# Performance work log

Measured on AMD Instinct MI355X. Metric: run time of the kernel, lower is better.

Reference implementation:

```python
import jax, jax.numpy as jnp
import numpy as np

EPS = 1e-5  # torch BatchNorm1d default eps

N_NODES = 100000
N_EDGES = 1250000
N_GRAPHS = 512
F_IN = 16
HID = 64


def _bn(x, w, b):
    # track_running_stats=False, momentum=None -> always batch statistics (biased var)
    m = jnp.mean(x, axis=0)
    v = jnp.var(x, axis=0)
    return (x - m) * jax.lax.rsqrt(v + EPS) * w + b


def _prelu(x, a):
    return jnp.where(x >= 0, x, a * x)


def _gcn_conv(x, W, b, src, dst, n):
    # PyG GCNConv: h = x W; add self loops; sym-norm by deg^-1/2 on target degrees
    h = x @ W  # [N, out]
    ones = jnp.ones(src.shape[0], x.dtype)
    deg = jax.ops.segment_sum(ones, dst, num_segments=n) + 1.0  # +1 self loop
    dis = jax.lax.rsqrt(deg)  # deg >= 1 so finite
    norm = (dis[src] * dis[dst])[:, None]  # [E,1]
    agg = jax.ops.segment_sum(h[src] * norm, dst, num_segments=n)
    # self-loop contribution: norm = dis[i]*dis[i]
    return agg + h * (dis * dis)[:, None] + b


def setup_inputs() -> dict:
    key = jax.random.key(0)
    ks = jax.random.split(key, 12)
    x = jax.random.normal(ks[0], (N_NODES, F_IN), dtype=jnp.float32)
    edge_index = jax.random.randint(ks[1], (2, N_EDGES), 0, N_NODES, dtype=jnp.int32)
    # evenly spaced graph ids so every segment is non-empty (global_max_pool)
    batch = ((jnp.arange(N_NODES, dtype=jnp.int32) * N_GRAPHS) // N_NODES).astype(jnp.int32)
    s = 0.1
    W1 = jax.random.normal(ks[2], (F_IN, HID), jnp.float32) * s
    b1 = jnp.zeros((HID,), jnp.float32)
    W2 = jax.random.normal(ks[3], (HID, HID), jnp.float32) * s
    b2 = jnp.zeros((HID,), jnp.float32)
    lw1 = jax.random.normal(ks[4], (HID, HID), jnp.float32) * s
    lb1 = jnp.zeros((HID,), jnp.float32)
    lw2 = jax.random.normal(ks[5], (HID, 1), jnp.float32) * s
    lb2 = jnp.zeros((1,), jnp.float32)
    bn1_w = jnp.ones((HID,), jnp.float32); bn1_b = jnp.zeros((HID,), jnp.float32)
    bn2_w = jnp.ones((HID,), jnp.float32); bn2_b = jnp.zeros((HID,), jnp.float32)
    bn3_w = jnp.ones((HID,), jnp.float32); bn3_b = jnp.zeros((HID,), jnp.float32)
    bn4_w = jnp.ones((1,), jnp.float32); bn4_b = jnp.zeros((1,), jnp.float32)
    a1 = jnp.full((1,), 0.25, jnp.float32)
    a2 = jnp.full((1,), 0.25, jnp.float32)
    a3 = jnp.full((1,), 0.25, jnp.float32)
    a4 = jnp.full((1,), 0.25, jnp.float32)
    return {"x": x, "edge_index": edge_index, "batch": batch,
            "W1": W1, "b1": b1, "W2": W2, "b2": b2,
            "bn1_w": bn1_w, "bn1_b": bn1_b, "bn2_w": bn2_w, "bn2_b": bn2_b,
            "bn3_w": bn3_w, "bn3_b": bn3_b, "bn4_w": bn4_w, "bn4_b": bn4_b,
            "lw1": lw1, "lb1": lb1, "lw2": lw2, "lb2": lb2,
            "a1": a1, "a2": a2, "a3": a3, "a4": a4}


def reference(x, edge_index, batch, W1, b1, W2, b2,
              bn1_w, bn1_b, bn2_w, bn2_b, bn3_w, bn3_b, bn4_w, bn4_b,
              lw1, lb1, lw2, lb2, a1, a2, a3, a4):
    src, dst = edge_index[0], edge_index[1]
    n = x.shape[0]
    h = _gcn_conv(x, W1, b1, src, dst, n)
    h = _prelu(_bn(h, bn1_w, bn1_b), a1)
    h = _gcn_conv(h, W2, b2, src, dst, n)
    h = _prelu(_bn(h, bn2_w, bn2_b), a2)
    g = jax.ops.segment_max(h, batch, num_segments=N_GRAPHS)  # global_max_pool
    g = _prelu(_bn(g @ lw1 + lb1, bn3_w, bn3_b), a3)
    g = _prelu(_bn(g @ lw2 + lb2, bn4_w, bn4_b), a4)
    return g
```

## Files before the change

### kernel.cpp

```cpp
#include <hip/hip_runtime.h>
#include <hip/hip_bf16.h>

#define N_NODES 100000
#define N_EDGES 1250000
#define N_GRAPHS 512
#define F_IN 16
#define HID 64
#define EPS 1e-5f

#define K_B 1563
#define B_H 250
#define EPB 5000
#define M_SC (K_B * B_H)

typedef unsigned int uint;

__device__ __forceinline__ uint f2bf(float f) {
    uint u = __float_as_uint(f);
    return (u + 0x7fffu + ((u >> 16) & 1u)) >> 16;
}
__device__ __forceinline__ uint pack2(float lo, float hi) {
    return f2bf(lo) | (f2bf(hi) << 16);
}
__device__ __forceinline__ void unpack8(float* o, uint4 v) {
    o[0] = __uint_as_float(v.x << 16); o[1] = __uint_as_float(v.x & 0xffff0000u);
    o[2] = __uint_as_float(v.y << 16); o[3] = __uint_as_float(v.y & 0xffff0000u);
    o[4] = __uint_as_float(v.z << 16); o[5] = __uint_as_float(v.z & 0xffff0000u);
    o[6] = __uint_as_float(v.w << 16); o[7] = __uint_as_float(v.w & 0xffff0000u);
}
__device__ __forceinline__ void accum8(float* a, uint4 v) {
    a[0] += __uint_as_float(v.x << 16); a[1] += __uint_as_float(v.x & 0xffff0000u);
    a[2] += __uint_as_float(v.y << 16); a[3] += __uint_as_float(v.y & 0xffff0000u);
    a[4] += __uint_as_float(v.z << 16); a[5] += __uint_as_float(v.z & 0xffff0000u);
    a[6] += __uint_as_float(v.w << 16); a[7] += __uint_as_float(v.w & 0xffff0000u);
}


__global__ __launch_bounds__(256) void k_hist(const int4* __restrict__ dst4,
                                              int* __restrict__ hist) {
    __shared__ int h[K_B];
    int t = threadIdx.x, b = blockIdx.x;
    for (int k = t; k < K_B; k += 256) h[k] = 0;
    __syncthreads();
    const int4* d4 = dst4 + b * (EPB / 4);
    for (int i = t; i < EPB / 4; i += 256) {
        int4 d = d4[i];
        atomicAdd(&h[d.x >> 6], 1);
        atomicAdd(&h[d.y >> 6], 1);
        atomicAdd(&h[d.z >> 6], 1);
        atomicAdd(&h[d.w >> 6], 1);
    }
    __syncthreads();
    for (int k = t; k < K_B; k += 256) hist[k * B_H + b] = h[k];
}

__global__ void k_s1(const int* __restrict__ in, int* __restrict__ out,
                     int* __restrict__ bsum, int n) {
    __shared__ int sh[256];
    int blk = blockIdx.x, t = threadIdx.x;
    int base = blk * 1024 + t * 4;
    int v[4];
#pragma unroll
    for (int j = 0; j < 4; j++) { int i = base + j; v[j] = (i < n) ? in[i] : 0; }
    int tsum = v[0] + v[1] + v[2] + v[3];
    sh[t] = tsum;
    __syncthreads();
    for (int ofs = 1; ofs < 256; ofs <<= 1) {
        int x = (t >= ofs) ? sh[t - ofs] : 0;
        __syncthreads();
        sh[t] += x;
        __syncthreads();
    }
    int run = sh[t] - tsum;
    if (t == 255) bsum[blk] = sh[255];
#pragma unroll
    for (int j = 0; j < 4; j++) { int i = base + j; if (i < n) out[i] = run; run += v[j]; }
}

__global__ void k_s2(int* __restrict__ bsum, int nb) {
    __shared__ int sh[512];
    int t = threadIdx.x;
    int v = (t < nb) ? bsum[t] : 0;
    sh[t] = v;
    __syncthreads();
    for (int ofs = 1; ofs < 512; ofs <<= 1) {
        int x = (t >= ofs) ? sh[t - ofs] : 0;
        __syncthreads();
        sh[t] += x;
        __syncthreads();
    }
    if (t < nb) bsum[t] = sh[t] - v;
}

__global__ void k_s3(int* __restrict__ out, const int* __restrict__ bsum, int n) {
    int i = blockIdx.x * 256 + threadIdx.x;
    if (i < n) out[i] += bsum[i >> 10];
}

__global__ __launch_bounds__(256) void k_bucketize(const int4* __restrict__ src4,
        const int4* __restrict__ dst4, const int* __restrict__ ebase,
        int* __restrict__ ebuck) {
    __shared__ int base[K_B];
    int t = threadIdx.x, b = blockIdx.x;
    for (int k = t; k < K_B; k += 256) base[k] = ebase[k * B_H + b];
    __syncthreads();
    const int4* s4 = src4 + b * (EPB / 4);
    const int4* d4 = dst4 + b * (EPB / 4);
    for (int i = t; i < EPB / 4; i += 256) {
        int4 s = s4[i];
        int4 d = d4[i];
        int p;
        p = atomicAdd(&base[d.x >> 6], 1); ebuck[p] = s.x | ((d.x & 63) << 17);
        p = atomicAdd(&base[d.y >> 6], 1); ebuck[p] = s.y | ((d.y & 63) << 17);
        p = atomicAdd(&base[d.z >> 6], 1); ebuck[p] = s.z | ((d.z & 63) << 17);
        p = atomicAdd(&base[d.w >> 6], 1); ebuck[p] = s.w | ((d.w & 63) << 17);
    }
}

__global__ __launch_bounds__(256) void k_csr(const int* __restrict__ ebase,
        const int* __restrict__ ebuck, int* __restrict__ col,
        int2* __restrict__ meta, float* __restrict__ dis) {
    int k = blockIdx.x, t = threadIdx.x;
    int beg = ebase[k * B_H];
    int end = (k + 1 < K_B) ? ebase[(k + 1) * B_H] : N_EDGES;
    int m = end - beg;
    __shared__ int c[64];
    __shared__ int sb[64];
    if (t < 64) c[t] = 0;
    __syncthreads();
    for (int i = t; i < m; i += 256) atomicAdd(&c[ebuck[beg + i] >> 17], 1);
    __syncthreads();
    if (t < 64) {
        int v = c[t];
        int incl = v;
#pragma unroll
        for (int o = 1; o < 64; o <<= 1) { int u = __shfl_up(incl, o); if (t >= o) incl += u; }
        int excl = incl - v;
        int node = k * 64 + t;
        if (node < N_NODES) {
            meta[node] = make_int2(beg + excl, v);
            dis[node] = rsqrtf((float)v + 1.0f);
        }
        sb[t] = beg + excl;
    }
    __syncthreads();
    for (int i = t; i < m; i += 256) {
        int e = ebuck[beg + i];
        int pos = atomicAdd(&sb[e >> 17], 1);
        col[pos] = e & 0x1FFFF;
    }
}


__global__ __launch_bounds__(512) void k_gemm1(const float* __restrict__ x,
        const float* __restrict__ W1, const float* __restrict__ dis,
        ushort* __restrict__ A) {
    __shared__ float Ws[F_IN * HID];
    __shared__ float xs[32 * F_IN];
    int t = threadIdx.x;
    Ws[t] = W1[t];
    Ws[t + 512] = W1[t + 512];
    int n0 = blockIdx.x * 32;
    xs[t] = x[n0 * F_IN + t];
    __syncthreads();
    int f = t & 63, w = t >> 6;
    float Wreg[F_IN];
#pragma unroll
    for (int k = 0; k < F_IN; k++) Wreg[k] = Ws[k * HID + f];
#pragma unroll
    for (int i = 0; i < 4; i++) {
        int nl = w * 4 + i;
        float acc = 0.f;
#pragma unroll
        for (int kq = 0; kq < 4; kq++) {
            const float4 xv = *(const float4*)&xs[nl * F_IN + kq * 4];
            acc = fmaf(xv.x, Wreg[4 * kq + 0], acc);
            acc = fmaf(xv.y, Wreg[4 * kq + 1], acc);
            acc = fmaf(xv.z, Wreg[4 * kq + 2], acc);
            acc = fmaf(xv.w, Wreg[4 * kq + 3], acc);
        }
        int n = n0 + nl;
        A[(size_t)n * HID + f] = (ushort)f2bf(acc * dis[n]);
    }
}

__global__ __launch_bounds__(512) void k_gemm2(const ushort* __restrict__ B,
        const float* __restrict__ scale, const float* __restrict__ shift,
        const float* __restrict__ alpha, const float* __restrict__ W2,
        const float* __restrict__ dis, ushort* __restrict__ A2) {
    __shared__ float Ws[HID * HID];
    __shared__ float xs[32 * HID];
    int t = threadIdx.x;
#pragma unroll
    for (int i = 0; i < 8; i++) Ws[i * 512 + t] = W2[i * 512 + t];
    int n0 = blockIdx.x * 32;
    float al = alpha[0];
    {
        const uint* Bu = (const uint*)(B + (size_t)n0 * HID);
#pragma unroll
        for (int i = 0; i < 2; i++) {
            int idx = i * 512 + t;
            uint u = Bu[idx];
            int fp = (idx & 31) * 2;
            int row = idx >> 5;
            float lo = __uint_as_float(u << 16) * scale[fp] + shift[fp];
            float hi = __uint_as_float(u & 0xffff0000u) * scale[fp + 1] + shift[fp + 1];
            lo = lo >= 0.f ? lo : al * lo;
            hi = hi >= 0.f ? hi : al * hi;
            xs[row * HID + fp] = lo;
            xs[row * HID + fp + 1] = hi;
        }
    }
    __syncthreads();
    int f = t & 63, w = t >> 6;
    float Wreg[HID];
#pragma unroll
    for (int k = 0; k < HID; k++) Wreg[k] = Ws[k * HID + f];
#pragma unroll
    for (int i = 0; i < 4; i++) {
        int nl = w * 4 + i;
        float acc = 0.f;
#pragma unroll
        for (int kq = 0; kq < 16; kq++) {
            const float4 xv = *(const float4*)&xs[nl * HID + kq * 4];
            acc = fmaf(xv.x, Wreg[4 * kq + 0], acc);
            acc = fmaf(xv.y, Wreg[4 * kq + 1], acc);
            acc = fmaf(xv.z, Wreg[4 * kq + 2], acc);
            acc = fmaf(xv.w, Wreg[4 * kq + 3], acc);
        }
        int n = n0 + nl;
        A2[(size_t)n * HID + f] = (ushort)f2bf(acc * dis[n]);
    }
}

__global__ __launch_bounds__(256) void k_agg(const uint4* __restrict__ Asc,
        const float* __restrict__ dis, const int2* __restrict__ meta,
        const int* __restrict__ col, const float* __restrict__ bias,
        uint4* __restrict__ outB) {
    int t = threadIdx.x;
    int nid = blockIdx.x * 32 + (t >> 3);
    int fq = t & 7;
    int2 mt = meta[nid];
    int beg = mt.x, m = mt.y;
    float acc[8] = {0, 0, 0, 0, 0, 0, 0, 0};
    int j = 0;
    for (; j + 2 <= m; j += 2) {
        int s0 = col[beg + j];
        int s1 = col[beg + j + 1];
        uint4 r0 = Asc[(size_t)s0 * 8 + fq];
        uint4 r1 = Asc[(size_t)s1 * 8 + fq];
        accum8(acc, r0);
        accum8(acc, r1);
    }
    if (j < m) {
        int s = col[beg + j];
        accum8(acc, Asc[(size_t)s * 8 + fq]);
    }
    accum8(acc, Asc[(size_t)nid * 8 + fq]);
    float dn = dis[nid];
    float4 b0 = ((const float4*)bias)[fq * 2];
    float4 b1 = ((const float4*)bias)[fq * 2 + 1];
    float o0 = b0.x + dn * acc[0], o1 = b0.y + dn * acc[1];
    float o2 = b0.z + dn * acc[2], o3 = b0.w + dn * acc[3];
    float o4 = b1.x + dn * acc[4], o5 = b1.y + dn * acc[5];
    float o6 = b1.z + dn * acc[6], o7 = b1.w + dn * acc[7];
    uint4 ov;
    ov.x = pack2(o0, o1); ov.y = pack2(o2, o3);
    ov.z = pack2(o4, o5); ov.w = pack2(o6, o7);
    outB[(size_t)nid * 8 + fq] = ov;
}

__global__ __launch_bounds__(256) void k_stats(const uint4* __restrict__ a,
        float* __restrict__ sum, float* __restrict__ sumsq) {
    int t = threadIdx.x, rg = t >> 3, fq = t & 7;
    float s[8] = {0, 0, 0, 0, 0, 0, 0, 0}, q[8] = {0, 0, 0, 0, 0, 0, 0, 0};
    for (int r = blockIdx.x * 32 + rg; r < N_NODES; r += gridDim.x * 32) {
        float o[8];
        unpack8(o, a[(size_t)r * 8 + fq]);
#pragma unroll
        for (int i = 0; i < 8; i++) { s[i] += o[i]; q[i] += o[i] * o[i]; }
    }
    __shared__ float shs[2048], shq[2048];
#pragma unroll
    for (int i = 0; i < 8; i++) {
        shs[rg * 64 + fq * 8 + i] = s[i];
        shq[rg * 64 + fq * 8 + i] = q[i];
    }
    __syncthreads();
    if (t < 64) {
        float ts = 0, tq = 0;
#pragma unroll
        for (int i = 0; i < 32; i++) { ts += shs[i * 64 + t]; tq += shq[i * 64 + t]; }
        atomicAdd(&sum[t], ts);
        atomicAdd(&sumsq[t], tq);
    }
}

__global__ void k_bnfin(const float* __restrict__ sum, const float* __restrict__ sumsq,
                        const float* __restrict__ w, const float* __restrict__ b,
                        float* __restrict__ scale, float* __restrict__ shift, float invn) {
    int f = threadIdx.x;
    float m = sum[f] * invn;
    float v = sumsq[f] * invn - m * m;
    float sc = w[f] * rsqrtf(v + EPS);
    scale[f] = sc;
    shift[f] = b[f] - m * sc;
}

__global__ __launch_bounds__(256) void k_pool(const uint4* __restrict__ a,
        const float* __restrict__ scale, const float* __restrict__ shift,
        const float* __restrict__ alpha, float* __restrict__ g) {
    int gi = blockIdx.x;
    int lo = (gi * N_NODES + N_GRAPHS - 1) / N_GRAPHS;
    int hi = ((gi + 1) * N_NODES + N_GRAPHS - 1) / N_GRAPHS;
    int t = threadIdx.x, rg = t >> 3, fq = t & 7;
    float al = alpha[0];
    float4 c0 = ((const float4*)scale)[fq * 2], c1 = ((const float4*)scale)[fq * 2 + 1];
    float4 d0 = ((const float4*)shift)[fq * 2], d1 = ((const float4*)shift)[fq * 2 + 1];
    float sc[8] = {c0.x, c0.y, c0.z, c0.w, c1.x, c1.y, c1.z, c1.w};
    float sh[8] = {d0.x, d0.y, d0.z, d0.w, d1.x, d1.y, d1.z, d1.w};
    float mx[8];
#pragma unroll
    for (int i = 0; i < 8; i++) mx[i] = -INFINITY;
    for (int r = lo + rg; r < hi; r += 32) {
        float o[8];
        unpack8(o, a[(size_t)r * 8 + fq]);
#pragma unroll
        for (int i = 0; i < 8; i++) {
            float v = o[i] * sc[i] + sh[i];
            v = v >= 0.f ? v : al * v;
            mx[i] = fmaxf(mx[i], v);
        }
    }
    __shared__ float sm[2048];
#pragma unroll
    for (int i = 0; i < 8; i++) sm[rg * 64 + fq * 8 + i] = mx[i];
    __syncthreads();
    if (t < 64) {
        float m = sm[t];
#pragma unroll
        for (int i = 1; i < 32; i++) m = fmaxf(m, sm[i * 64 + t]);
        g[gi * HID + t] = m;
    }
}

__global__ void k_lin1(const float* __restrict__ g, const float* __restrict__ lw1,
                       const float* __restrict__ lb1, float* __restrict__ t1,
                       float* __restrict__ s3, float* __restrict__ ss3) {
    __shared__ float row[HID];
    int r = blockIdx.x, f = threadIdx.x;
    row[f] = g[r * HID + f];
    __syncthreads();
    float acc = lb1[f];
#pragma unroll
    for (int k = 0; k < HID; k++) acc += row[k] * lw1[k * HID + f];
    t1[r * HID + f] = acc;
    atomicAdd(&s3[f], acc);
    atomicAdd(&ss3[f], acc * acc);
}

__global__ void k_lin2(const float* __restrict__ t1, const float* __restrict__ s3,
                       const float* __restrict__ ss3, const float* __restrict__ bn3w,
                       const float* __restrict__ bn3b, const float* __restrict__ a3,
                       const float* __restrict__ lw2, const float* __restrict__ lb2,
                       float* __restrict__ t2, float* __restrict__ s4) {
    int r = blockIdx.x, f = threadIdx.x;
    const float invn = 1.f / N_GRAPHS;
    float m = s3[f] * invn;
    float v = ss3[f] * invn - m * m;
    float sc = bn3w[f] * rsqrtf(v + EPS);
    float x = (t1[r * HID + f] - m) * sc + bn3b[f];
    float al = a3[0];
    x = (x >= 0.f) ? x : al * x;
    float p = x * lw2[f];
    for (int o = 32; o > 0; o >>= 1) p += __shfl_down(p, o);
    if (f == 0) {
        float tv = p + lb2[0];
        t2[r] = tv;
        atomicAdd(&s4[0], tv);
        atomicAdd(&s4[1], tv * tv);
    }
}

__global__ void k_final(const float* __restrict__ t2, const float* __restrict__ s4,
                        const float* __restrict__ bn4w, const float* __restrict__ bn4b,
                        const float* __restrict__ a4, float* __restrict__ out) {
    int r = threadIdx.x;
    const float invn = 1.f / N_GRAPHS;
    float m = s4[0] * invn;
    float v = s4[1] * invn - m * m;
    float sc = bn4w[0] * rsqrtf(v + EPS);
    float x = (t2[r] - m) * sc + bn4b[0];
    float al = a4[0];
    out[r] = (x >= 0.f) ? x : al * x;
}

extern "C" void kernel_launch(void* const* d_in, const int* in_sizes, int n_in,
                              void* d_out, int out_size, void* d_ws, size_t ws_size,
                              hipStream_t stream) {
    const float* x   = (const float*)d_in[0];
    const int*   ei  = (const int*)d_in[1];
    const int4*  src4 = (const int4*)ei;
    const int4*  dst4 = (const int4*)(ei + N_EDGES);
    const float* W1  = (const float*)d_in[3];
    const float* b1  = (const float*)d_in[4];
    const float* W2  = (const float*)d_in[5];
    const float* b2  = (const float*)d_in[6];
    const float* bn1w = (const float*)d_in[7];
    const float* bn1b = (const float*)d_in[8];
    const float* bn2w = (const float*)d_in[9];
    const float* bn2b = (const float*)d_in[10];
    const float* bn3w = (const float*)d_in[11];
    const float* bn3b = (const float*)d_in[12];
    const float* bn4w = (const float*)d_in[13];
    const float* bn4b = (const float*)d_in[14];
    const float* lw1  = (const float*)d_in[15];
    const float* lb1  = (const float*)d_in[16];
    const float* lw2  = (const float*)d_in[17];
    const float* lb2  = (const float*)d_in[18];
    const float* a1   = (const float*)d_in[19];
    const float* a2   = (const float*)d_in[20];
    const float* a3   = (const float*)d_in[21];
    const float* a4   = (const float*)d_in[22];
    float* out = (float*)d_out;

    char* p = (char*)d_ws;
    auto carve = [&](size_t bytes) -> void* {
        void* r = (void*)p;
        p += (bytes + 255) & ~(size_t)255;
        return r;
    };
    int*    hist = (int*)carve((size_t)M_SC * 4);
    int*    ebase = (int*)carve((size_t)M_SC * 4);
    int*    ebuck = (int*)carve((size_t)N_EDGES * 4);
    int*    col  = (int*)carve((size_t)N_EDGES * 4);
    float*  dis  = (float*)carve((size_t)N_NODES * 4);
    int2*   meta = (int2*)carve((size_t)N_NODES * 8);
    int*    bsum = (int*)carve(2048);
    ushort* A    = (ushort*)carve((size_t)N_NODES * HID * 2);
    ushort* B    = (ushort*)carve((size_t)N_NODES * HID * 2);
    float*  gbuf = (float*)carve((size_t)N_GRAPHS * HID * 4);
    float*  t1   = (float*)carve((size_t)N_GRAPHS * HID * 4);
    float*  t2   = (float*)carve((size_t)N_GRAPHS * 4);
    float*  stats = (float*)carve(16 * HID * 4);
    float* s1 = stats,        *ss1 = stats + 64;
    float* sc1 = stats + 128, *sh1 = stats + 192;
    float* s2 = stats + 256,  *ss2 = stats + 320;
    float* sc2 = stats + 384, *sh2 = stats + 448;
    float* s3 = stats + 512,  *ss3 = stats + 576;
    float* s4 = stats + 640;

    hipMemsetAsync(stats, 0, 16 * HID * 4, stream);

    const int SC_BLKS = (M_SC + 1023) / 1024;

    k_hist<<<B_H, 256, 0, stream>>>(dst4, hist);
    k_s1<<<SC_BLKS, 256, 0, stream>>>(hist, ebase, bsum, M_SC);
    k_s2<<<1, 512, 0, stream>>>(bsum, SC_BLKS);
    k_s3<<<(M_SC + 255) / 256, 256, 0, stream>>>(ebase, bsum, M_SC);
    k_bucketize<<<B_H, 256, 0, stream>>>(src4, dst4, ebase, ebuck);
    k_csr<<<K_B, 256, 0, stream>>>(ebase, ebuck, col, meta, dis);

    const int NB32 = N_NODES / 32;
    k_gemm1<<<NB32, 512, 0, stream>>>(x, W1, dis, A);
    k_agg<<<NB32, 256, 0, stream>>>((const uint4*)A, dis, meta, col, b1, (uint4*)B);
    k_stats<<<512, 256, 0, stream>>>((const uint4*)B, s1, ss1);
    k_bnfin<<<1, 64, 0, stream>>>(s1, ss1, bn1w, bn1b, sc1, sh1, 1.f / N_NODES);
    k_gemm2<<<NB32, 512, 0, stream>>>(B, sc1, sh1, a1, W2, dis, A);
    k_agg<<<NB32, 256, 0, stream>>>((const uint4*)A, dis, meta, col, b2, (uint4*)B);
    k_stats<<<512, 256, 0, stream>>>((const uint4*)B, s2, ss2);
    k_bnfin<<<1, 64, 0, stream>>>(s2, ss2, bn2w, bn2b, sc2, sh2, 1.f / N_NODES);
    k_pool<<<N_GRAPHS, 256, 0, stream>>>((const uint4*)B, sc2, sh2, a2, gbuf);
    k_lin1<<<N_GRAPHS, 64, 0, stream>>>(gbuf, lw1, lb1, t1, s3, ss3);
    k_lin2<<<N_GRAPHS, 64, 0, stream>>>(t1, s3, ss3, bn3w, bn3b, a3, lw2, lb2, t2, s4);
    k_final<<<1, N_GRAPHS, 0, stream>>>(t2, s4, bn4w, bn4b, a4, out);
}
```

Measured before the change: 208.9 us.

## Fuse BN stats into aggregation, fold scan fixup and head kernels

Removes the k_s3 scan-fixup pass by adding the block offsets inside bucketize and csr. BatchNorm sum and sum-of-squares are now reduced inside k_agg and written to 8 replicated atomic slots, which drops the separate stats and bnfin kernels. BN finalisation is recomputed per block in gemm2 and pool. The lin1 layer is folded into pool, and lin2 plus the final BN go into a single head kernel. The aggregation loop is unrolled to 4 edges. Together this cuts several kernel launches and one full re-read of the node features, at the cost of atomics and redundant per-block BN finalisation.

```diff
diff --git a/kernel.cpp b/kernel.cpp
--- a/kernel.cpp
+++ b/kernel.cpp
@@ -92,17 +92,15 @@
     if (t < nb) bsum[t] = sh[t] - v;
 }
 
-__global__ void k_s3(int* __restrict__ out, const int* __restrict__ bsum, int n) {
-    int i = blockIdx.x * 256 + threadIdx.x;
-    if (i < n) out[i] += bsum[i >> 10];
-}
-
 __global__ __launch_bounds__(256) void k_bucketize(const int4* __restrict__ src4,
         const int4* __restrict__ dst4, const int* __restrict__ ebase,
-        int* __restrict__ ebuck) {
+        const int* __restrict__ bsum, int* __restrict__ ebuck) {
     __shared__ int base[K_B];
     int t = threadIdx.x, b = blockIdx.x;
-    for (int k = t; k < K_B; k += 256) base[k] = ebase[k * B_H + b];
+    for (int k = t; k < K_B; k += 256) {
+        int idx = k * B_H + b;
+        base[k] = ebase[idx] + bsum[idx >> 10];
+    }
     __syncthreads();
     const int4* s4 = src4 + b * (EPB / 4);
     const int4* d4 = dst4 + b * (EPB / 4);
@@ -118,11 +116,18 @@
 }
 
 __global__ __launch_bounds__(256) void k_csr(const int* __restrict__ ebase,
-        const int* __restrict__ ebuck, int* __restrict__ col,
-        int2* __restrict__ meta, float* __restrict__ dis) {
+        const int* __restrict__ bsum, const int* __restrict__ ebuck,
+        int* __restrict__ col, int2* __restrict__ meta, float* __restrict__ dis) {
     int k = blockIdx.x, t = threadIdx.x;
-    int beg = ebase[k * B_H];
-    int end = (k + 1 < K_B) ? ebase[(k + 1) * B_H] : N_EDGES;
+    int i0 = k * B_H;
+    int beg = ebase[i0] + bsum[i0 >> 10];
+    int end;
+    if (k + 1 < K_B) {
+        int i1 = (k + 1) * B_H;
+        end = ebase[i1] + bsum[i1 >> 10];
+    } else {
+        end = N_EDGES;
+    }
     int m = end - beg;
     __shared__ int c[64];
     __shared__ int sb[64];
@@ -185,14 +190,28 @@
 }
 
 __global__ __launch_bounds__(512) void k_gemm2(const ushort* __restrict__ B,
-        const float* __restrict__ scale, const float* __restrict__ shift,
+        const float* __restrict__ s1r, const float* __restrict__ ss1r,
+        const float* __restrict__ bnw, const float* __restrict__ bnb,
         const float* __restrict__ alpha, const float* __restrict__ W2,
         const float* __restrict__ dis, ushort* __restrict__ A2) {
     __shared__ float Ws[HID * HID];
     __shared__ float xs[32 * HID];
+    __shared__ float scs[64], shsv[64];
     int t = threadIdx.x;
 #pragma unroll
     for (int i = 0; i < 8; i++) Ws[i * 512 + t] = W2[i * 512 + t];
+    if (t < 64) {
+        float s = 0, q = 0;
+#pragma unroll
+        for (int r = 0; r < 8; r++) { s += s1r[r * 64 + t]; q += ss1r[r * 64 + t]; }
+        const float invn = 1.f / N_NODES;
+        float m = s * invn;
+        float v = q * invn - m * m;
+        float sc = bnw[t] * rsqrtf(v + EPS);
+        scs[t] = sc;
+        shsv[t] = bnb[t] - m * sc;
+    }
+    __syncthreads();
     int n0 = blockIdx.x * 32;
     float al = alpha[0];
     {
@@ -203,8 +222,8 @@
             uint u = Bu[idx];
             int fp = (idx & 31) * 2;
             int row = idx >> 5;
-            float lo = __uint_as_float(u << 16) * scale[fp] + shift[fp];
-            float hi = __uint_as_float(u & 0xffff0000u) * scale[fp + 1] + shift[fp + 1];
+            float lo = __uint_as_float(u << 16) * scs[fp] + shsv[fp];
+            float hi = __uint_as_float(u & 0xffff0000u) * scs[fp + 1] + shsv[fp + 1];
             lo = lo >= 0.f ? lo : al * lo;
             hi = hi >= 0.f ? hi : al * hi;
             xs[row * HID + fp] = lo;
@@ -236,7 +255,8 @@
 __global__ __launch_bounds__(256) void k_agg(const uint4* __restrict__ Asc,
         const float* __restrict__ dis, const int2* __restrict__ meta,
         const int* __restrict__ col, const float* __restrict__ bias,
-        uint4* __restrict__ outB) {
+        uint4* __restrict__ outB, float* __restrict__ sumr,
+        float* __restrict__ sumsqr) {
     int t = threadIdx.x;
     int nid = blockIdx.x * 32 + (t >> 3);
     int fq = t & 7;
@@ -244,15 +264,21 @@
     int beg = mt.x, m = mt.y;
     float acc[8] = {0, 0, 0, 0, 0, 0, 0, 0};
     int j = 0;
-    for (; j + 2 <= m; j += 2) {
+    for (; j + 4 <= m; j += 4) {
         int s0 = col[beg + j];
         int s1 = col[beg + j + 1];
+        int s2 = col[beg + j + 2];
+        int s3 = col[beg + j + 3];
         uint4 r0 = Asc[(size_t)s0 * 8 + fq];
         uint4 r1 = Asc[(size_t)s1 * 8 + fq];
+        uint4 r2 = Asc[(size_t)s2 * 8 + fq];
+        uint4 r3 = Asc[(size_t)s3 * 8 + fq];
         accum8(acc, r0);
         accum8(acc, r1);
-    }
-    if (j < m) {
+        accum8(acc, r2);
+        accum8(acc, r3);
+    }
+    for (; j < m; ++j) {
         int s = col[beg + j];
         accum8(acc, Asc[(size_t)s * 8 + fq]);
     }
@@ -260,65 +286,75 @@
     float dn = dis[nid];
     float4 b0 = ((const float4*)bias)[fq * 2];
     float4 b1 = ((const float4*)bias)[fq * 2 + 1];
-    float o0 = b0.x + dn * acc[0], o1 = b0.y + dn * acc[1];
-    float o2 = b0.z + dn * acc[2], o3 = b0.w + dn * acc[3];
-    float o4 = b1.x + dn * acc[4], o5 = b1.y + dn * acc[5];
-    float o6 = b1.z + dn * acc[6], o7 = b1.w + dn * acc[7];
+    float o[8];
+    o[0] = b0.x + dn * acc[0]; o[1] = b0.y + dn * acc[1];
+    o[2] = b0.z + dn * acc[2]; o[3] = b0.w + dn * acc[3];
+    o[4] = b1.x + dn * acc[4]; o[5] = b1.y + dn * acc[5];
+    o[6] = b1.z + dn * acc[6]; o[7] = b1.w + dn * acc[7];
     uint4 ov;
-    ov.x = pack2(o0, o1); ov.y = pack2(o2, o3);
-    ov.z = pack2(o4, o5); ov.w = pack2(o6, o7);
+    ov.x = pack2(o[0], o[1]); ov.y = pack2(o[2], o[3]);
+    ov.z = pack2(o[4], o[5]); ov.w = pack2(o[6], o[7]);
     outB[(size_t)nid * 8 + fq] = ov;
-}
-
-__global__ __launch_bounds__(256) void k_stats(const uint4* __restrict__ a,
-        float* __restrict__ sum, float* __restrict__ sumsq) {
+
+    float sq[8];
+#pragma unroll
+    for (int i = 0; i < 8; i++) sq[i] = o[i] * o[i];
+#pragma unroll
+    for (int ofs = 8; ofs <= 32; ofs <<= 1) {
+#pragma unroll
+        for (int i = 0; i < 8; i++) {
+            o[i] += __shfl_xor(o[i], ofs);
+            sq[i] += __shfl_xor(sq[i], ofs);
+        }
+    }
+    __shared__ float ps[4][64], pq[4][64];
+    int w = t >> 6, lane = t & 63;
+    if (lane < 8) {
+#pragma unroll
+        for (int i = 0; i < 8; i++) {
+            ps[w][lane * 8 + i] = o[i];
+            pq[w][lane * 8 + i] = sq[i];
+        }
+    }
+    __syncthreads();
+    if (t < 64) {
+        float a = ps[0][t] + ps[1][t] + ps[2][t] + ps[3][t];
+        float b = pq[0][t] + pq[1][t] + pq[2][t] + pq[3][t];
+        int rep = (blockIdx.x & 7) * 64;
+        atomicAdd(&sumr[rep + t], a);
+        atomicAdd(&sumsqr[rep + t], b);
+    }
+}
+
+__global__ __launch_bounds__(256) void k_pool(const uint4* __restrict__ a,
+        const float* __restrict__ s2r, const float* __restrict__ ss2r,
+        const float* __restrict__ bnw, const float* __restrict__ bnb,
+        const float* __restrict__ alpha, const float* __restrict__ lw1,
+        const float* __restrict__ lb1, float* __restrict__ th,
+        float* __restrict__ s3r, float* __restrict__ ss3r) {
+    __shared__ float scs[64], shsv[64];
+    __shared__ float sm[2048];
+    __shared__ float gr[64];
+    int gi = blockIdx.x;
     int t = threadIdx.x, rg = t >> 3, fq = t & 7;
-    float s[8] = {0, 0, 0, 0, 0, 0, 0, 0}, q[8] = {0, 0, 0, 0, 0, 0, 0, 0};
-    for (int r = blockIdx.x * 32 + rg; r < N_NODES; r += gridDim.x * 32) {
-        float o[8];
-        unpack8(o, a[(size_t)r * 8 + fq]);
-#pragma unroll
-        for (int i = 0; i < 8; i++) { s[i] += o[i]; q[i] += o[i] * o[i]; }
-    }
-    __shared__ float shs[2048], shq[2048];
-#pragma unroll
-    for (int i = 0; i < 8; i++) {
-        shs[rg * 64 + fq * 8 + i] = s[i];
-        shq[rg * 64 + fq * 8 + i] = q[i];
-    }
-    __syncthreads();
     if (t < 64) {
-        float ts = 0, tq = 0;
-#pragma unroll
-        for (int i = 0; i < 32; i++) { ts += shs[i * 64 + t]; tq += shq[i * 64 + t]; }
-        atomicAdd(&sum[t], ts);
-        atomicAdd(&sumsq[t], tq);
-    }
-}
-
-__global__ void k_bnfin(const float* __restrict__ sum, const float* __restrict__ sumsq,
-                        const float* __restrict__ w, const float* __restrict__ b,
-                        float* __restrict__ scale, float* __restrict__ shift, float invn) {
-    int f = threadIdx.x;
-    float m = sum[f] * invn;
-    float v = sumsq[f] * invn - m * m;
-    float sc = w[f] * rsqrtf(v + EPS);
-    scale[f] = sc;
-    shift[f] = b[f] - m * sc;
-}
-
-__global__ __launch_bounds__(256) void k_pool(const uint4* __restrict__ a,
-        const float* __restrict__ scale, const float* __restrict__ shift,
-        const float* __restrict__ alpha, float* __restrict__ g) {
-    int gi = blockIdx.x;
+        float s = 0, q = 0;
+#pragma unroll
+        for (int r = 0; r < 8; r++) { s += s2r[r * 64 + t]; q += ss2r[r * 64 + t]; }
+        const float invn = 1.f / N_NODES;
+        float m = s * invn;
+        float v = q * invn - m * m;
+        float sc = bnw[t] * rsqrtf(v + EPS);
+        scs[t] = sc;
+        shsv[t] = bnb[t] - m * sc;
+    }
+    __syncthreads();
     int lo = (gi * N_NODES + N_GRAPHS - 1) / N_GRAPHS;
     int hi = ((gi + 1) * N_NODES + N_GRAPHS - 1) / N_GRAPHS;
-    int t = threadIdx.x, rg = t >> 3, fq = t & 7;
     float al = alpha[0];
-    float4 c0 = ((const float4*)scale)[fq * 2], c1 = ((const float4*)scale)[fq * 2 + 1];
-    float4 d0 = ((const float4*)shift)[fq * 2], d1 = ((const float4*)shift)[fq * 2 + 1];
-    float sc[8] = {c0.x, c0.y, c0.z, c0.w, c1.x, c1.y, c1.z, c1.w};
-    float sh[8] = {d0.x, d0.y, d0.z, d0.w, d1.x, d1.y, d1.z, d1.w};
+    float sc[8], sh[8];
+#pragma unroll
+    for (int i = 0; i < 8; i++) { sc[i] = scs[fq * 8 + i]; sh[i] = shsv[fq * 8 + i]; }
     float mx[8];
 #pragma unroll
     for (int i = 0; i < 8; i++) mx[i] = -INFINITY;
@@ -332,7 +368,6 @@
             mx[i] = fmaxf(mx[i], v);
         }
     }
-    __shared__ float sm[2048];
 #pragma unroll
     for (int i = 0; i < 8; i++) sm[rg * 64 + fq * 8 + i] = mx[i];
     __syncthreads();
@@ -340,59 +375,65 @@
         float m = sm[t];
 #pragma unroll
         for (int i = 1; i < 32; i++) m = fmaxf(m, sm[i * 64 + t]);
-        g[gi * HID + t] = m;
-    }
-}
-
-__global__ void k_lin1(const float* __restrict__ g, const float* __restrict__ lw1,
-                       const float* __restrict__ lb1, float* __restrict__ t1,
-                       float* __restrict__ s3, float* __restrict__ ss3) {
-    __shared__ float row[HID];
-    int r = blockIdx.x, f = threadIdx.x;
-    row[f] = g[r * HID + f];
-    __syncthreads();
-    float acc = lb1[f];
-#pragma unroll
-    for (int k = 0; k < HID; k++) acc += row[k] * lw1[k * HID + f];
-    t1[r * HID + f] = acc;
-    atomicAdd(&s3[f], acc);
-    atomicAdd(&ss3[f], acc * acc);
-}
-
-__global__ void k_lin2(const float* __restrict__ t1, const float* __restrict__ s3,
-                       const float* __restrict__ ss3, const float* __restrict__ bn3w,
-                       const float* __restrict__ bn3b, const float* __restrict__ a3,
-                       const float* __restrict__ lw2, const float* __restrict__ lb2,
-                       float* __restrict__ t2, float* __restrict__ s4) {
-    int r = blockIdx.x, f = threadIdx.x;
+        gr[t] = m;
+    }
+    __syncthreads();
+    if (t < 64) {
+        float acc = lb1[t];
+#pragma unroll
+        for (int k = 0; k < 64; k++) acc = fmaf(gr[k], lw1[k * 64 + t], acc);
+        th[gi * 64 + t] = acc;
+        int rep = (gi & 7) * 64;
+        atomicAdd(&s3r[rep + t], acc);
+        atomicAdd(&ss3r[rep + t], acc * acc);
+    }
+}
+
+__global__ __launch_bounds__(512) void k_head(const float* __restrict__ th,
+        const float* __restrict__ s3r, const float* __restrict__ ss3r,
+        const float* __restrict__ bn3w, const float* __restrict__ bn3b,
+        const float* __restrict__ a3, const float* __restrict__ lw2,
+        const float* __restrict__ lb2, const float* __restrict__ bn4w,
+        const float* __restrict__ bn4b, const float* __restrict__ a4,
+        float* __restrict__ out) {
+    int t = threadIdx.x, w = t >> 6, lane = t & 63;
+    __shared__ float t2s[N_GRAPHS];
+    __shared__ float rs[8], rq[8];
     const float invn = 1.f / N_GRAPHS;
-    float m = s3[f] * invn;
-    float v = ss3[f] * invn - m * m;
-    float sc = bn3w[f] * rsqrtf(v + EPS);
-    float x = (t1[r * HID + f] - m) * sc + bn3b[f];
-    float al = a3[0];
-    x = (x >= 0.f) ? x : al * x;
-    float p = x * lw2[f];
-    for (int o = 32; o > 0; o >>= 1) p += __shfl_down(p, o);
-    if (f == 0) {
-        float tv = p + lb2[0];
-        t2[r] = tv;
-        atomicAdd(&s4[0], tv);
-        atomicAdd(&s4[1], tv * tv);
-    }
-}
-
-__global__ void k_final(const float* __restrict__ t2, const float* __restrict__ s4,
-                        const float* __restrict__ bn4w, const float* __restrict__ bn4b,
-                        const float* __restrict__ a4, float* __restrict__ out) {
-    int r = threadIdx.x;
-    const float invn = 1.f / N_GRAPHS;
-    float m = s4[0] * invn;
-    float v = s4[1] * invn - m * m;
-    float sc = bn4w[0] * rsqrtf(v + EPS);
-    float x = (t2[r] - m) * sc + bn4b[0];
-    float al = a4[0];
-    out[r] = (x >= 0.f) ? x : al * x;
+    float s = 0, q = 0;
+#pragma unroll
+    for (int r = 0; r < 8; r++) { s += s3r[r * 64 + lane]; q += ss3r[r * 64 + lane]; }
+    float m3 = s * invn;
+    float v3 = q * invn - m3 * m3;
+    float sc3 = bn3w[lane] * rsqrtf(v3 + EPS);
+    float sh3 = bn3b[lane] - m3 * sc3;
+    float al3 = a3[0];
+    float wv = lw2[lane];
+    float lb = lb2[0];
+    for (int r = w; r < N_GRAPHS; r += 8) {
+        float xv = th[r * 64 + lane] * sc3 + sh3;
+        xv = xv >= 0.f ? xv : al3 * xv;
+        float p = xv * wv;
+#pragma unroll
+        for (int o = 32; o > 0; o >>= 1) p += __shfl_xor(p, o);
+        if (lane == 0) t2s[r] = p + lb;
+    }
+    __syncthreads();
+    float tv = t2s[t];
+    float ps = tv, pq = tv * tv;
+#pragma unroll
+    for (int o = 32; o > 0; o >>= 1) { ps += __shfl_xor(ps, o); pq += __shfl_xor(pq, o); }
+    if (lane == 0) { rs[w] = ps; rq[w] = pq; }
+    __syncthreads();
+    float S = 0, Q = 0;
+#pragma unroll
+    for (int i = 0; i < 8; i++) { S += rs[i]; Q += rq[i]; }
+    float m4 = S * invn;
+    float v4 = Q * invn - m4 * m4;
+    float sc4 = bn4w[0] * rsqrtf(v4 + EPS);
+    float xb = (tv - m4) * sc4 + bn4b[0];
+    float al4 = a4[0];
+    out[t] = xb >= 0.f ? xb : al4 * xb;
 }
 
 extern "C" void kernel_launch(void* const* d_in, const int* in_sizes, int n_in,
@@ -439,39 +480,31 @@
     int*    bsum = (int*)carve(2048);
     ushort* A    = (ushort*)carve((size_t)N_NODES * HID * 2);
     ushort* B    = (ushort*)carve((size_t)N_NODES * HID * 2);
-    float*  gbuf = (float*)carve((size_t)N_GRAPHS * HID * 4);
-    float*  t1   = (float*)carve((size_t)N_GRAPHS * HID * 4);
-    float*  t2   = (float*)carve((size_t)N_GRAPHS * 4);
-    float*  stats = (float*)carve(16 * HID * 4);
-    float* s1 = stats,        *ss1 = stats + 64;
-    float* sc1 = stats + 128, *sh1 = stats + 192;
-    float* s2 = stats + 256,  *ss2 = stats + 320;
-    float* sc2 = stats + 384, *sh2 = stats + 448;
-    float* s3 = stats + 512,  *ss3 = stats + 576;
-    float* s4 = stats + 640;
-
-    hipMemsetAsync(stats, 0, 16 * HID * 4, stream);
+    float*  th   = (float*)carve((size_t)N_GRAPHS * HID * 4);
+    float*  statsr = (float*)carve(6 * 512 * 4);
+    float* s1r = statsr,          *ss1r = statsr + 512;
+    float* s2r = statsr + 1024,   *ss2r = statsr + 1536;
+    float* s3r = statsr + 2048,   *ss3r = statsr + 2560;
+
+    hipMemsetAsync(statsr, 0, 6 * 512 * 4, stream);
 
     const int SC_BLKS = (M_SC + 1023) / 1024;
 
     k_hist<<<B_H, 256, 0, stream>>>(dst4, hist);
     k_s1<<<SC_BLKS, 256, 0, stream>>>(hist, ebase, bsum, M_SC);
     k_s2<<<1, 512, 0, stream>>>(bsum, SC_BLKS);
-    k_s3<<<(M_SC + 255) / 256, 256, 0, stream>>>(ebase, bsum, M_SC);
-    k_bucketize<<<B_H, 256, 0, stream>>>(src4, dst4, ebase, ebuck);
-    k_csr<<<K_B, 256, 0, stream>>>(ebase, ebuck, col, meta, dis);
+    k_bucketize<<<B_H, 256, 0, stream>>>(src4, dst4, ebase, bsum, ebuck);
+    k_csr<<<K_B, 256, 0, stream>>>(ebase, bsum, ebuck, col, meta, dis);
 
     const int NB32 = N_NODES / 32;
     k_gemm1<<<NB32, 512, 0, stream>>>(x, W1, dis, A);
-    k_agg<<<NB32, 256, 0, stream>>>((const uint4*)A, dis, meta, col, b1, (uint4*)B);
-    k_stats<<<512, 256, 0, stream>>>((const uint4*)B, s1, ss1);
-    k_bnfin<<<1, 64, 0, stream>>>(s1, ss1, bn1w, bn1b, sc1, sh1, 1.f / N_NODES);
-    k_gemm2<<<NB32, 512, 0, stream>>>(B, sc1, sh1, a1, W2, dis, A);
-    k_agg<<<NB32, 256, 0, stream>>>((const uint4*)A, dis, meta, col, b2, (uint4*)B);
-    k_stats<<<512, 256, 0, stream>>>((const uint4*)B, s2, ss2);
-    k_bnfin<<<1, 64, 0, stream>>>(s2, ss2, bn2w, bn2b, sc2, sh2, 1.f / N_NODES);
-    k_pool<<<N_GRAPHS, 256, 0, stream>>>((const uint4*)B, sc2, sh2, a2, gbuf);
-    k_lin1<<<N_GRAPHS, 64, 0, stream>>>(gbuf, lw1, lb1, t1, s3, ss3);
-    k_lin2<<<N_GRAPHS, 64, 0, stream>>>(t1, s3, ss3, bn3w, bn3b, a3, lw2, lb2, t2, s4);
-    k_final<<<1, N_GRAPHS, 0, stream>>>(t2, s4, bn4w, bn4b, a4, out);
-}
+    k_agg<<<NB32, 256, 0, stream>>>((const uint4*)A, dis, meta, col, b1, (uint4*)B,
+                                    s1r, ss1r);
+    k_gemm2<<<NB32, 512, 0, stream>>>(B, s1r, ss1r, bn1w, bn1b, a1, W2, dis, A);
+    k_agg<<<NB32, 256, 0, stream>>>((const uint4*)A, dis, meta, col, b2, (uint4*)B,
+                                    s2r, ss2r);
+    k_pool<<<N_GRAPHS, 256, 0, stream>>>((const uint4*)B, s2r, ss2r, bn2w, bn2b, a2,
+                                         lw1, lb1, th, s3r, ss3r);
+    k_head<<<1, 512, 0, stream>>>(th, s3r, ss3r, bn3w, bn3b, a3, lw2, lb2,
+                                  bn4w, bn4b, a4, out);
+}
```

Result: faster. 181.5 us (-13.1%).
